# Kernel tuning notes

Measured on AMD Instinct MI355X. Metric: run time of the kernel, lower is better.

Reference implementation:

```python
import jax, jax.numpy as jnp
import numpy as np

EXPERT_CAPACITY = 1024  # per-batch per-expert capacity (token_priority <= capacity)


def setup_inputs() -> dict:
    key = jax.random.key(0)
    ks = jax.random.split(key, 5)
    B, S, D, FF, E = 2, 4096, 1024, 4096, 8
    return {
        "hidden_states": jax.random.normal(ks[0], (B, S, D), dtype=jnp.float32),
        "gate_w": jax.random.normal(ks[1], (D, E), dtype=jnp.float32) * (1.0 / np.sqrt(D)),
        "w1": jax.random.normal(ks[2], (E, D, FF), dtype=jnp.float32) * (1.0 / np.sqrt(D)),
        "w2": jax.random.normal(ks[3], (E, FF, D), dtype=jnp.float32) * (1.0 / np.sqrt(FF)),
        "w3": jax.random.normal(ks[4], (E, D, FF), dtype=jnp.float32) * (1.0 / np.sqrt(D)),
    }


def reference(hidden_states, gate_w, w1, w2, w3):
    B, S, D = hidden_states.shape
    E = gate_w.shape[1]
    C = EXPERT_CAPACITY

    # ---- route (jitter_noise = 0) ----
    router_logits = jnp.einsum("bsd,de->bse", hidden_states, gate_w)  # [B,S,E]
    router_probs = jax.nn.softmax(router_logits, axis=-1)
    sel = jnp.argmax(router_probs, axis=-1)  # [B,S] top-1 expert
    onehot = jax.nn.one_hot(sel, E, dtype=jnp.int32)  # [B,S,E]
    priority = jnp.cumsum(onehot, axis=1)  # cumsum over sequence (dim=-2)
    # position of token in its chosen expert's buffer (0-based)
    pos = jnp.take_along_axis(priority, sel[..., None], axis=-1)[..., 0] - 1  # [B,S]
    keep = pos < C  # token_priority <= expert_capacity
    max_prob = jnp.max(router_probs, axis=-1, keepdims=True)  # [B,S,1]

    # ---- dispatch: scatter kept tokens into [B,E,C,D]; dropped tokens have pos>=C -> mode='drop'
    b_idx = jnp.broadcast_to(jnp.arange(B)[:, None], (B, S))
    buf = jnp.zeros((B, E, C, D), dtype=hidden_states.dtype)
    buf = buf.at[b_idx, sel, pos].set(hidden_states, mode="drop")

    # ---- per-expert gated MLP (grouped GEMM): act(x@w1) * (x@w3) @ w2 ----
    g = jax.nn.silu(jnp.einsum("becd,edf->becf", buf, w1))
    u = jnp.einsum("becd,edf->becf", buf, w3)
    expert_out = jnp.einsum("becf,efd->becd", g * u, w2)  # [B,E,C,D]

    # ---- combine: kept tokens get expert output, dropped tokens keep hidden_states ----
    pos_g = jnp.minimum(pos, C - 1)  # safe gather index for dropped tokens
    gathered = expert_out[b_idx, sel, pos_g]  # [B,S,D]
    next_states = jnp.where(keep[..., None], gathered, hidden_states)
    out = max_prob * next_states  # dropout is identity (p=0)
    return out, router_logits
```

## Files before the change

### kernel.cpp

```cpp
#include <hip/hip_runtime.h>
#include <hip/hip_bf16.h>
#include <stdint.h>

#define B_  2
#define S_  4096
#define D_  1024
#define FF_ 4096
#define E_  8
#define C_  1024

typedef unsigned short u16;
typedef unsigned int   u32;
typedef float f32x4  __attribute__((ext_vector_type(4)));
typedef short bf16x8 __attribute__((ext_vector_type(8)));
typedef u16   u16x8  __attribute__((ext_vector_type(8)));

static __device__ __forceinline__ u16 f2bf(float f) {
    union { float f; u32 u; } v; v.f = f;
    u32 u = v.u;
    u32 r = (u + 0x7FFFu + ((u >> 16) & 1u)) >> 16;
    return (u16)r;
}

static __device__ __forceinline__ void gload_lds16(const u16* g, u16* l) {
    __builtin_amdgcn_global_load_lds(
        (const __attribute__((address_space(1))) u32*)g,
        (__attribute__((address_space(3))) u32*)l, 16, 0, 0);
}

#define BAR()    asm volatile("s_barrier" ::: "memory")
#define WAITV(n) asm volatile("s_waitcnt vmcnt(" #n ")" ::: "memory")
#define WAITL0() do { asm volatile("s_waitcnt lgkmcnt(0)" ::: "memory"); \
                      __builtin_amdgcn_sched_barrier(0); } while (0)

__global__ __launch_bounds__(256) void transpose_cvt(const float* __restrict__ src,
                                                     u16* __restrict__ dst, int K, int N) {
    __shared__ u16 t[64 * 64];
    size_t mat = (size_t)blockIdx.z * K * N;
    int n0 = blockIdx.x * 64, k0 = blockIdx.y * 64;
    int l = threadIdx.x & 63, w = threadIdx.x >> 6;
#pragma unroll
    for (int p = 0; p < 2; ++p) {
        int k = p * 32 + w * 8 + ((l >> 4) << 1);
        int n = (l & 15) * 4;
        float4 v0 = *(const float4*)&src[mat + (size_t)(k0 + k) * N + n0 + n];
        float4 v1 = *(const float4*)&src[mat + (size_t)(k0 + k + 1) * N + n0 + n];
        float a0[4] = {v0.x, v0.y, v0.z, v0.w};
        float a1[4] = {v1.x, v1.y, v1.z, v1.w};
#pragma unroll
        for (int j = 0; j < 4; ++j) {
            int nn = n + j;
            u32 pk = (u32)f2bf(a0[j]) | ((u32)f2bf(a1[j]) << 16);
            int slot = (k >> 3) ^ ((nn & 7) ^ ((nn >> 3) & 7));
            *(u32*)((char*)t + nn * 128 + slot * 16 + (k & 7) * 2) = pk;
        }
    }
    __syncthreads();
#pragma unroll
    for (int p = 0; p < 2; ++p) {
        int n = p * 32 + (threadIdx.x >> 3);
        int k8 = threadIdx.x & 7;
        int slot = k8 ^ ((n & 7) ^ ((n >> 3) & 7));
        u16x8 v = *(u16x8*)((char*)t + n * 128 + slot * 16);
        *(u16x8*)&dst[mat + (size_t)(n0 + n) * K + k0 + k8 * 8] = v;
    }
}

__global__ __launch_bounds__(256) void router_kernel(const float* __restrict__ hidden,
                                                     const float* __restrict__ gate_w,
                                                     float* __restrict__ logits_out,
                                                     int* __restrict__ sel,
                                                     float* __restrict__ maxp) {
    __shared__ float gw[D_ * E_];
    for (int i = threadIdx.x; i < D_ * E_ / 4; i += 256)
        ((float4*)gw)[i] = ((const float4*)gate_w)[i];
    __syncthreads();

    int wave = threadIdx.x >> 6, lane = threadIdx.x & 63;
    int tok = blockIdx.x * 4 + wave;
    const float* hrow = hidden + (size_t)tok * D_;

    double acc[8] = {0, 0, 0, 0, 0, 0, 0, 0};
#pragma unroll 4
    for (int i = 0; i < D_ / 64; i++) {
        int d = i * 64 + lane;
        float h = hrow[d];
        const float4* g4 = (const float4*)(gw + d * 8);
        float4 g0 = g4[0], g1 = g4[1];
        acc[0] += (double)h * g0.x; acc[1] += (double)h * g0.y;
        acc[2] += (double)h * g0.z; acc[3] += (double)h * g0.w;
        acc[4] += (double)h * g1.x; acc[5] += (double)h * g1.y;
        acc[6] += (double)h * g1.z; acc[7] += (double)h * g1.w;
    }
#pragma unroll
    for (int off = 32; off > 0; off >>= 1)
#pragma unroll
        for (int e = 0; e < 8; e++)
            acc[e] += __shfl_xor(acc[e], off);

    float l[8];
#pragma unroll
    for (int e = 0; e < 8; e++) l[e] = (float)acc[e];
    if (lane < 8) logits_out[(size_t)tok * 8 + lane] = l[lane];

    int am = 0; float mx = l[0];
#pragma unroll
    for (int e = 1; e < 8; e++) if (l[e] > mx) { mx = l[e]; am = e; }
    float sum = 0.f;
#pragma unroll
    for (int e = 0; e < 8; e++) sum += expf(l[e] - mx);
    if (lane == 0) { sel[tok] = am; maxp[tok] = 1.0f / sum; }
}

__global__ __launch_bounds__(1024) void scan_kernel(const int* __restrict__ sel,
                                                    int* __restrict__ pos,
                                                    int* __restrict__ slot_token,
                                                    int* __restrict__ counts) {
    __shared__ int hist[16][8];
    __shared__ int base[16][8];
    int b = blockIdx.x;
    int tid = threadIdx.x, wv = tid >> 6, l = tid & 63;
    unsigned long long below = (l == 0) ? 0ull : ((~0ull) >> (64 - l));
    const int* sb = sel + b * S_;

    int eloc[4];
    int cnt[8] = {0, 0, 0, 0, 0, 0, 0, 0};
#pragma unroll
    for (int c = 0; c < 4; c++) {
        int s = wv * 256 + c * 64 + l;
        int e = sb[s];
        eloc[c] = e;
#pragma unroll
        for (int ex = 0; ex < 8; ex++)
            cnt[ex] += (int)__popcll(__ballot(e == ex));
    }
    if (l == 0)
#pragma unroll
        for (int ex = 0; ex < 8; ex++) hist[wv][ex] = cnt[ex];
    __syncthreads();
    if (tid < 128) {
        int ex = tid & 7, v = tid >> 3;
        int s = 0;
        for (int w2 = 0; w2 < v; w2++) s += hist[w2][ex];
        base[v][ex] = s;
        if (v == 15) {
            int tot = s + hist[15][ex];
            counts[b * 8 + ex] = tot < C_ ? tot : C_;
        }
    }
    __syncthreads();
    int carry[8];
#pragma unroll
    for (int ex = 0; ex < 8; ex++) carry[ex] = base[wv][ex];
#pragma unroll
    for (int c = 0; c < 4; c++) {
        int s = wv * 256 + c * 64 + l;
        int e = eloc[c];
        int p = 0;
#pragma unroll
        for (int ex = 0; ex < 8; ex++) {
            unsigned long long m = __ballot(e == ex);
            if (e == ex) p = carry[ex] + (int)__popcll(m & below);
            carry[ex] += (int)__popcll(m);
        }
        pos[b * S_ + s] = p;
        if (p < C_) slot_token[(b * E_ + e) * C_ + p] = s;
    }
}

__global__ __launch_bounds__(256) void gather_kernel(const float* __restrict__ hidden,
                                                     const int* __restrict__ slot_token,
                                                     const int* __restrict__ counts,
                                                     u16* __restrict__ xg) {
    int z = blockIdx.x >> 8;
    int r0 = (blockIdx.x & 255) * 4;
    int cnt = counts[z];
    int slot = r0 + (threadIdx.x >> 6);
    if (slot >= cnt) return;
    int l = threadIdx.x & 63;
    int b = z >> 3;
    int tok = slot_token[z * C_ + slot];
    const float4* src = (const float4*)(hidden + (size_t)(b * S_ + tok) * D_) + l * 4;
    u16x8* dst = (u16x8*)(xg + ((size_t)z * C_ + slot) * D_) + l * 2;
#pragma unroll
    for (int h = 0; h < 2; h++) {
        float4 a = src[h * 2], c = src[h * 2 + 1];
        u16x8 o;
        o[0] = f2bf(a.x); o[1] = f2bf(a.y); o[2] = f2bf(a.z); o[3] = f2bf(a.w);
        o[4] = f2bf(c.x); o[5] = f2bf(c.y); o[6] = f2bf(c.z); o[7] = f2bf(c.w);
        dst[h] = o;
    }
}

__global__ __launch_bounds__(256, 2) void gemm1_kernel(const u16* __restrict__ xg,
                                                       const u16* __restrict__ w1t,
                                                       const u16* __restrict__ w3t,
                                                       const int* __restrict__ counts,
                                                       u16* __restrict__ hbuf) {
    extern __shared__ u16 lds[];
    int phys = blockIdx.x;
    int virt = (phys & 7) * 512 + (phys >> 3);
    int by = virt & 7, bx = (virt >> 3) & 31, bz = virt >> 8;

    int z = bz;
    int cnt = counts[z];
    int c0 = by * 128;
    if (c0 >= cnt) return;
    int n0 = bx * 128;
    int e = z & 7;

    int tid = threadIdx.x, wn = tid >> 6, l = tid & 63;

    const u16* pA[2];
#pragma unroll
    for (int i = 0; i < 2; i++) {
        int q = i * 256 + tid;
        int r = q >> 2, pc = q & 3;
        pA[i] = xg + ((size_t)z * C_ + c0 + r) * D_ + (pc ^ ((r >> 1) & 3)) * 8;
    }
    const u16* pB[4];
#pragma unroll
    for (int i = 0; i < 4; i++) {
        int q = i * 256 + tid;
        int R = q >> 2, pc = q & 3;
        int panel = (R >> 5) & 1;
        int ffl = ((R >> 6) << 5) + (R & 31);
        const u16* wmat = panel ? w3t : w1t;
        pB[i] = wmat + ((size_t)e * FF_ + n0 + ffl) * D_ + (pc ^ ((R >> 1) & 3)) * 8;
    }
    u32 dA = (u32)tid * 8;
    u32 dB = 4096 + (u32)tid * 8;

    u32 ck = (u32)(((l >> 4) ^ ((l >> 1) & 3)) * 8);

    f32x4 acc[8][4] = {};

    auto STAGE = [&](int t) {
        u16* Ls = lds + (t % 3) * 12288;
        int ko = t << 5;
#pragma unroll
        for (int i = 0; i < 2; i++) gload_lds16(pA[i] + ko, Ls + dA + i * 2048);
#pragma unroll
        for (int i = 0; i < 4; i++) gload_lds16(pB[i] + ko, Ls + dB + i * 2048);
    };

    constexpr int NK = D_ / 32;
    STAGE(0); STAGE(1);
    for (int t = 0; t < NK; ++t) {
        if (t + 1 < NK) { WAITV(6); } else { WAITV(0); }
        BAR();
        const u16* Ls = lds + (t % 3) * 12288;
        bf16x8 af[8], bf[4];
#pragma unroll
        for (int f = 0; f < 8; f++)
            af[f] = *(const bf16x8*)(Ls + (u32)(f * 16 + (l & 15)) * 32 + ck);
#pragma unroll
        for (int j = 0; j < 4; j++)
            bf[j] = *(const bf16x8*)(Ls + 4096 + (u32)(wn * 64 + j * 16 + (l & 15)) * 32 + ck);
        if (t + 2 < NK) STAGE(t + 2);
        WAITL0();
        __builtin_amdgcn_s_setprio(1);
#pragma unroll
        for (int f = 0; f < 8; f++)
#pragma unroll
            for (int j = 0; j < 4; j++)
                acc[f][j] = __builtin_amdgcn_mfma_f32_16x16x32_bf16(af[f], bf[j], acc[f][j], 0, 0, 0);
        __builtin_amdgcn_s_setprio(0);
    }

#pragma unroll
    for (int f = 0; f < 8; f++) {
        int rb = c0 + f * 16 + ((l >> 4) << 2);
#pragma unroll
        for (int j = 0; j < 2; j++) {
            int ff = n0 + wn * 32 + j * 16 + (l & 15);
#pragma unroll
            for (int r = 0; r < 4; r++) {
                int slot = rb + r;
                if (slot < cnt) {
                    float g = acc[f][j][r], uu = acc[f][j + 2][r];
                    float h = (g / (1.f + __expf(-g))) * uu;
                    hbuf[((size_t)z * C_ + slot) * FF_ + ff] = f2bf(h);
                }
            }
        }
    }
}

__global__ __launch_bounds__(512, 2) void gemm2_kernel(const u16* __restrict__ hbuf,
                                                       const u16* __restrict__ w2t,
                                                       const int* __restrict__ slot_token,
                                                       const int* __restrict__ counts,
                                                       const float* __restrict__ maxp,
                                                       float* __restrict__ out) {
    extern __shared__ u16 lds[];
    int phys = blockIdx.x + 4 * (blockIdx.y + 4 * blockIdx.z);
    int virt = (phys & 7) * 32 + (phys >> 3);
    int bx = virt & 3, by = (virt >> 2) & 3, bz = virt >> 4;

    int z = bz;
    int cnt = counts[z];
    int c0 = by * 256;
    if (c0 >= cnt) return;
    int n0 = bx * 256;
    int b = z >> 3, e = z & 7;

    int tid = threadIdx.x, w = tid >> 6, l = tid & 63;
    int wm = w >> 2, wn = w & 3;

    int arow0 = tid >> 2;
    int lk = ((tid & 3) ^ ((tid >> 3) & 3)) * 8;
    const u16* pA0 = hbuf + ((size_t)z * C_ + c0 + arow0) * FF_ + lk;
    const u16* pA1 = pA0 + (size_t)128 * FF_;
    const u16* pB0 = w2t + ((size_t)e * D_ + n0 + arow0) * FF_ + lk;
    const u16* pB1 = pB0 + (size_t)128 * FF_;
    u32 wsl = (u32)tid * 8;

    u32 ck  = (u32)(((l >> 4) ^ ((l >> 1) & 3)) * 8);
    u32 aoff = (u32)(wm * 128 + (l & 15)) * 32 + ck;
    u32 boff = 8192 + (u32)(wn * 64 + (l & 15)) * 32 + ck;

    auto STAGE_A = [&](int t) {
        u16* Ls = lds + ((t & 3) << 14);
        int ko = t << 5;
        gload_lds16(pA0 + ko, Ls + wsl);
        gload_lds16(pA1 + ko, Ls + 4096 + wsl);
    };
    auto STAGE_B = [&](int t) {
        u16* Ls = lds + ((t & 3) << 14);
        int ko = t << 5;
        gload_lds16(pB0 + ko, Ls + 8192 + wsl);
        gload_lds16(pB1 + ko, Ls + 12288 + wsl);
    };

    f32x4 acc[8][4] = {};

    constexpr int NK = FF_ / 32;
    STAGE_A(0); STAGE_B(0); STAGE_A(1); STAGE_B(1); STAGE_A(2); STAGE_B(2);
    for (int t = 0; t < NK; ++t) {
        if (t + 2 < NK)      { WAITV(8); }
        else if (t + 1 < NK) { WAITV(4); }
        else                 { WAITV(0); }
        BAR();
        const u16* Ls = lds + ((t & 3) << 14);
        bf16x8 af[8], bfv[4];
#pragma unroll
        for (int f = 0; f < 4; f++) af[f] = *(const bf16x8*)(Ls + aoff + f * 512);
#pragma unroll
        for (int n = 0; n < 4; n++) bfv[n] = *(const bf16x8*)(Ls + boff + n * 512);
        if (t + 3 < NK) STAGE_A(t + 3);
        WAITL0();
        __builtin_amdgcn_s_setprio(1);
#pragma unroll
        for (int f = 0; f < 4; f++)
#pragma unroll
            for (int n = 0; n < 4; n++)
                acc[f][n] = __builtin_amdgcn_mfma_f32_16x16x32_bf16(af[f], bfv[n], acc[f][n], 0, 0, 0);
        __builtin_amdgcn_s_setprio(0);
        BAR();
#pragma unroll
        for (int f = 4; f < 8; f++) af[f] = *(const bf16x8*)(Ls + aoff + f * 512);
        if (t + 3 < NK) STAGE_B(t + 3);
        WAITL0();
        __builtin_amdgcn_s_setprio(1);
#pragma unroll
        for (int f = 4; f < 8; f++)
#pragma unroll
            for (int n = 0; n < 4; n++)
                acc[f][n] = __builtin_amdgcn_mfma_f32_16x16x32_bf16(af[f], bfv[n], acc[f][n], 0, 0, 0);
        __builtin_amdgcn_s_setprio(0);
    }

#pragma unroll
    for (int f = 0; f < 8; f++) {
        int row = wm * 128 + f * 16 + ((l >> 4) << 2);
#pragma unroll
        for (int rr = 0; rr < 4; rr++) {
            int slot = c0 + row + rr;
            if (slot < cnt) {
                int s = slot_token[z * C_ + slot];
                float sc = maxp[b * S_ + s];
                float* orow = out + ((size_t)b * S_ + s) * D_ + n0 + wn * 64 + (l & 15);
#pragma unroll
                for (int n = 0; n < 4; n++)
                    orow[n * 16] = sc * acc[f][n][rr];
            }
        }
    }
}

__global__ __launch_bounds__(256) void combine_dropped(const float* __restrict__ hidden,
                                                       const int* __restrict__ pos,
                                                       const float* __restrict__ maxp,
                                                       float* __restrict__ out) {
    int t = blockIdx.x;
    if (pos[t] < C_) return;
    float sc = maxp[t];
    const float* src = hidden + (size_t)t * D_;
    float* dst = out + (size_t)t * D_;
    for (int d = threadIdx.x; d < D_; d += 256) dst[d] = sc * src[d];
}

extern "C" void kernel_launch(void* const* d_in, const int* in_sizes, int n_in,
                              void* d_out, int out_size, void* d_ws, size_t ws_size,
                              hipStream_t stream) {
    const float* hidden = (const float*)d_in[0];
    const float* gate_w = (const float*)d_in[1];
    const float* w1     = (const float*)d_in[2];
    const float* w2     = (const float*)d_in[3];
    const float* w3     = (const float*)d_in[4];

    float* out        = (float*)d_out;
    float* logits_out = out + (size_t)B_ * S_ * D_;

    char* ws = (char*)d_ws;
    u16* xg        = (u16*)ws;            ws += (size_t)B_ * E_ * C_ * D_ * 2;
    u16* w1t       = (u16*)ws;            ws += (size_t)E_ * D_ * FF_ * 2;
    u16* w3t       = (u16*)ws;            ws += (size_t)E_ * D_ * FF_ * 2;
    u16* w2t       = (u16*)ws;            ws += (size_t)E_ * D_ * FF_ * 2;
    u16* hbuf      = (u16*)ws;            ws += (size_t)B_ * E_ * C_ * FF_ * 2;
    int*   sel        = (int*)ws;         ws += (size_t)B_ * S_ * 4;
    int*   pos        = (int*)ws;         ws += (size_t)B_ * S_ * 4;
    float* maxp       = (float*)ws;       ws += (size_t)B_ * S_ * 4;
    int*   slot_token = (int*)ws;         ws += (size_t)B_ * E_ * C_ * 4;
    int*   counts     = (int*)ws;         ws += (size_t)B_ * E_ * 4;

    (void)hipFuncSetAttribute((const void*)gemm1_kernel,
                              hipFuncAttributeMaxDynamicSharedMemorySize, 73728);
    (void)hipFuncSetAttribute((const void*)gemm2_kernel,
                              hipFuncAttributeMaxDynamicSharedMemorySize, 131072);

    router_kernel<<<B_ * S_ / 4, 256, 0, stream>>>(hidden, gate_w, logits_out, sel, maxp);
    scan_kernel<<<B_, 1024, 0, stream>>>(sel, pos, slot_token, counts);
    gather_kernel<<<B_ * E_ * 256, 256, 0, stream>>>(hidden, slot_token, counts, xg);

    transpose_cvt<<<dim3(FF_ / 64, D_ / 64, E_), 256, 0, stream>>>(w1, w1t, D_, FF_);
    transpose_cvt<<<dim3(FF_ / 64, D_ / 64, E_), 256, 0, stream>>>(w3, w3t, D_, FF_);
    transpose_cvt<<<dim3(D_ / 64, FF_ / 64, E_), 256, 0, stream>>>(w2, w2t, FF_, D_);

    gemm1_kernel<<<4096, 256, 73728, stream>>>(xg, w1t, w3t, counts, hbuf);
    gemm2_kernel<<<dim3(4, 4, 16), 512, 131072, stream>>>(hbuf, w2t, slot_token, counts, maxp, out);
    combine_dropped<<<B_ * S_, 256, 0, stream>>>(hidden, pos, maxp, out);
}
```

Baseline: 474.5 us.

## Make gemm1 a persistent kernel pulling tiles from an atomic work queue

Replaces the fixed 4096-block gemm1 grid with 512 persistent blocks that fetch tile indices from a global atomic counter. The scan kernel resets the counter. Tiles past an expert's token count are skipped cheaply inside the loop instead of costing a block launch. This is meant to improve load balance across CUs and cut launch and tail overhead, but it drops the previous XCD-aware block swizzle, adds atomic contention, and leaves a possible race on the shared item index when a block skips an empty tile.

New measurement: 682.6 us. 43.9% more time.

```diff
diff --git a/kernel.cpp b/kernel.cpp
--- a/kernel.cpp
+++ b/kernel.cpp
@@ -115,11 +115,13 @@
 __global__ __launch_bounds__(1024) void scan_kernel(const int* __restrict__ sel,
                                                     int* __restrict__ pos,
                                                     int* __restrict__ slot_token,
-                                                    int* __restrict__ counts) {
+                                                    int* __restrict__ counts,
+                                                    int* __restrict__ ctr) {
     __shared__ int hist[16][8];
     __shared__ int base[16][8];
     int b = blockIdx.x;
     int tid = threadIdx.x, wv = tid >> 6, l = tid & 63;
+    if (b == 0 && tid == 0) ctr[0] = 0;
     unsigned long long below = (l == 0) ? 0ull : ((~0ull) >> (64 - l));
     const int* sb = sel + b * S_;
 
@@ -192,95 +194,101 @@
     }
 }
 
+#define G1_NITEMS (16 * 32 * 8)
 __global__ __launch_bounds__(256, 2) void gemm1_kernel(const u16* __restrict__ xg,
                                                        const u16* __restrict__ w1t,
                                                        const u16* __restrict__ w3t,
                                                        const int* __restrict__ counts,
-                                                       u16* __restrict__ hbuf) {
+                                                       u16* __restrict__ hbuf,
+                                                       int* __restrict__ ctr) {
     extern __shared__ u16 lds[];
-    int phys = blockIdx.x;
-    int virt = (phys & 7) * 512 + (phys >> 3);
-    int by = virt & 7, bx = (virt >> 3) & 31, bz = virt >> 8;
-
-    int z = bz;
-    int cnt = counts[z];
-    int c0 = by * 128;
-    if (c0 >= cnt) return;
-    int n0 = bx * 128;
-    int e = z & 7;
+    __shared__ int s_item;
 
     int tid = threadIdx.x, wn = tid >> 6, l = tid & 63;
-
-    const u16* pA[2];
-#pragma unroll
-    for (int i = 0; i < 2; i++) {
-        int q = i * 256 + tid;
-        int r = q >> 2, pc = q & 3;
-        pA[i] = xg + ((size_t)z * C_ + c0 + r) * D_ + (pc ^ ((r >> 1) & 3)) * 8;
-    }
-    const u16* pB[4];
-#pragma unroll
-    for (int i = 0; i < 4; i++) {
-        int q = i * 256 + tid;
-        int R = q >> 2, pc = q & 3;
-        int panel = (R >> 5) & 1;
-        int ffl = ((R >> 6) << 5) + (R & 31);
-        const u16* wmat = panel ? w3t : w1t;
-        pB[i] = wmat + ((size_t)e * FF_ + n0 + ffl) * D_ + (pc ^ ((R >> 1) & 3)) * 8;
-    }
+    u32 ck = (u32)(((l >> 4) ^ ((l >> 1) & 3)) * 8);
     u32 dA = (u32)tid * 8;
     u32 dB = 4096 + (u32)tid * 8;
-
-    u32 ck = (u32)(((l >> 4) ^ ((l >> 1) & 3)) * 8);
-
-    f32x4 acc[8][4] = {};
-
-    auto STAGE = [&](int t) {
-        u16* Ls = lds + (t % 3) * 12288;
-        int ko = t << 5;
-#pragma unroll
-        for (int i = 0; i < 2; i++) gload_lds16(pA[i] + ko, Ls + dA + i * 2048);
-#pragma unroll
-        for (int i = 0; i < 4; i++) gload_lds16(pB[i] + ko, Ls + dB + i * 2048);
-    };
-
-    constexpr int NK = D_ / 32;
-    STAGE(0); STAGE(1);
-    for (int t = 0; t < NK; ++t) {
-        if (t + 1 < NK) { WAITV(6); } else { WAITV(0); }
-        BAR();
-        const u16* Ls = lds + (t % 3) * 12288;
-        bf16x8 af[8], bf[4];
-#pragma unroll
-        for (int f = 0; f < 8; f++)
-            af[f] = *(const bf16x8*)(Ls + (u32)(f * 16 + (l & 15)) * 32 + ck);
-#pragma unroll
-        for (int j = 0; j < 4; j++)
-            bf[j] = *(const bf16x8*)(Ls + 4096 + (u32)(wn * 64 + j * 16 + (l & 15)) * 32 + ck);
-        if (t + 2 < NK) STAGE(t + 2);
-        WAITL0();
-        __builtin_amdgcn_s_setprio(1);
-#pragma unroll
-        for (int f = 0; f < 8; f++)
+    int srcxor = ((tid & 3) ^ ((tid >> 3) & 3)) * 8;
+
+    for (;;) {
+        if (tid == 0) s_item = atomicAdd(ctr, 1);
+        __syncthreads();
+        int item = s_item;
+        if (item >= G1_NITEMS) break;
+        int cy = item & 7, ffx = (item >> 3) & 31, z = item >> 8;
+        int cnt = counts[z];
+        int c0 = cy * 128;
+        if (c0 >= cnt) continue;
+        int n0 = ffx * 128;
+        int e = z & 7;
+
+        const u16* pA[2];
+#pragma unroll
+        for (int i = 0; i < 2; i++) {
+            int q = i * 256 + tid;
+            int r = q >> 2;
+            pA[i] = xg + ((size_t)z * C_ + c0 + r) * D_ + srcxor;
+        }
+        const u16* pB[4];
+#pragma unroll
+        for (int i = 0; i < 4; i++) {
+            int q = i * 256 + tid;
+            int R = q >> 2;
+            int panel = (R >> 5) & 1;
+            int ffl = ((R >> 6) << 5) + (R & 31);
+            const u16* wmat = panel ? w3t : w1t;
+            pB[i] = wmat + ((size_t)e * FF_ + n0 + ffl) * D_ + srcxor;
+        }
+
+        f32x4 acc[8][4] = {};
+
+        auto STAGE = [&](int t) {
+            u16* Ls = lds + (t % 3) * 12288;
+            int ko = t << 5;
+#pragma unroll
+            for (int i = 0; i < 2; i++) gload_lds16(pA[i] + ko, Ls + dA + i * 2048);
+#pragma unroll
+            for (int i = 0; i < 4; i++) gload_lds16(pB[i] + ko, Ls + dB + i * 2048);
+        };
+
+        constexpr int NK = D_ / 32;
+        STAGE(0); STAGE(1);
+        for (int t = 0; t < NK; ++t) {
+            if (t + 1 < NK) { WAITV(6); } else { WAITV(0); }
+            BAR();
+            const u16* Ls = lds + (t % 3) * 12288;
+            bf16x8 af[8], bf[4];
+#pragma unroll
+            for (int f = 0; f < 8; f++)
+                af[f] = *(const bf16x8*)(Ls + (u32)(f * 16 + (l & 15)) * 32 + ck);
 #pragma unroll
             for (int j = 0; j < 4; j++)
-                acc[f][j] = __builtin_amdgcn_mfma_f32_16x16x32_bf16(af[f], bf[j], acc[f][j], 0, 0, 0);
-        __builtin_amdgcn_s_setprio(0);
-    }
-
-#pragma unroll
-    for (int f = 0; f < 8; f++) {
-        int rb = c0 + f * 16 + ((l >> 4) << 2);
-#pragma unroll
-        for (int j = 0; j < 2; j++) {
-            int ff = n0 + wn * 32 + j * 16 + (l & 15);
-#pragma unroll
-            for (int r = 0; r < 4; r++) {
-                int slot = rb + r;
-                if (slot < cnt) {
-                    float g = acc[f][j][r], uu = acc[f][j + 2][r];
-                    float h = (g / (1.f + __expf(-g))) * uu;
-                    hbuf[((size_t)z * C_ + slot) * FF_ + ff] = f2bf(h);
+                bf[j] = *(const bf16x8*)(Ls + 4096 + (u32)(wn * 64 + j * 16 + (l & 15)) * 32 + ck);
+            if (t + 2 < NK) STAGE(t + 2);
+            WAITL0();
+            __builtin_amdgcn_s_setprio(1);
+#pragma unroll
+            for (int f = 0; f < 8; f++)
+#pragma unroll
+                for (int j = 0; j < 4; j++)
+                    acc[f][j] = __builtin_amdgcn_mfma_f32_16x16x32_bf16(af[f], bf[j], acc[f][j], 0, 0, 0);
+            __builtin_amdgcn_s_setprio(0);
+        }
+
+#pragma unroll
+        for (int f = 0; f < 8; f++) {
+            int rb = c0 + f * 16 + ((l >> 4) << 2);
+#pragma unroll
+            for (int j = 0; j < 2; j++) {
+                int ff = n0 + wn * 32 + j * 16 + (l & 15);
+#pragma unroll
+                for (int r = 0; r < 4; r++) {
+                    int slot = rb + r;
+                    if (slot < cnt) {
+                        float g = acc[f][j][r], uu = acc[f][j + 2][r];
+                        float h = (g / (1.f + __expf(-g))) * uu;
+                        hbuf[((size_t)z * C_ + slot) * FF_ + ff] = f2bf(h);
+                    }
                 }
             }
         }
@@ -424,6 +432,7 @@
     float* maxp       = (float*)ws;       ws += (size_t)B_ * S_ * 4;
     int*   slot_token = (int*)ws;         ws += (size_t)B_ * E_ * C_ * 4;
     int*   counts     = (int*)ws;         ws += (size_t)B_ * E_ * 4;
+    int*   ctr        = (int*)ws;         ws += 256;
 
     (void)hipFuncSetAttribute((const void*)gemm1_kernel,
                               hipFuncAttributeMaxDynamicSharedMemorySize, 73728);
@@ -431,14 +440,14 @@
                               hipFuncAttributeMaxDynamicSharedMemorySize, 131072);
 
     router_kernel<<<B_ * S_ / 4, 256, 0, stream>>>(hidden, gate_w, logits_out, sel, maxp);
-    scan_kernel<<<B_, 1024, 0, stream>>>(sel, pos, slot_token, counts);
+    scan_kernel<<<B_, 1024, 0, stream>>>(sel, pos, slot_token, counts, ctr);
     gather_kernel<<<B_ * E_ * 256, 256, 0, stream>>>(hidden, slot_token, counts, xg);
 
     transpose_cvt<<<dim3(FF_ / 64, D_ / 64, E_), 256, 0, stream>>>(w1, w1t, D_, FF_);
     transpose_cvt<<<dim3(FF_ / 64, D_ / 64, E_), 256, 0, stream>>>(w3, w3t, D_, FF_);
     transpose_cvt<<<dim3(D_ / 64, FF_ / 64, E_), 256, 0, stream>>>(w2, w2t, FF_, D_);
 
-    gemm1_kernel<<<4096, 256, 73728, stream>>>(xg, w1t, w3t, counts, hbuf);
+    gemm1_kernel<<<512, 256, 73728, stream>>>(xg, w1t, w3t, counts, hbuf, ctr);
     gemm2_kernel<<<dim3(4, 4, 16), 512, 131072, stream>>>(hbuf, w2t, slot_token, counts, maxp, out);
     combine_dropped<<<B_ * S_, 256, 0, stream>>>(hidden, pos, maxp, out);
 }
```

## Enlarge gemm1 tile to 256x128 with 8 waves and k-64 double-buffered phases

Applied to the files above, without the earlier changes.

Rewrites the fused w1/w3 GEMM so each block of 512 threads computes a 256-token by 128-FF tile, with two M-waves sharing the B panel, instead of 128x128 with 4 waves. The K loop now steps by 64 in double-buffered LDS stages split into four phases. Each phase issues loads for the next stage while MFMAs run, and B fragments are reused across two phases. The aim is more reuse of weight loads and less global traffic per FLOP. In exchange it uses more LDS (128KB), allows one block per CU, adds extra barriers per phase, and wastes more work on partially filled capacity tiles.

Result: slower. 515.2 us (+8.6%).

```diff
diff --git a/kernel.cpp b/kernel.cpp
--- a/kernel.cpp
+++ b/kernel.cpp
@@ -192,93 +192,112 @@
     }
 }
 
-__global__ __launch_bounds__(256, 2) void gemm1_kernel(const u16* __restrict__ xg,
+__global__ __launch_bounds__(512, 1) void gemm1_kernel(const u16* __restrict__ xg,
                                                        const u16* __restrict__ w1t,
                                                        const u16* __restrict__ w3t,
                                                        const int* __restrict__ counts,
                                                        u16* __restrict__ hbuf) {
     extern __shared__ u16 lds[];
     int phys = blockIdx.x;
-    int virt = (phys & 7) * 512 + (phys >> 3);
-    int by = virt & 7, bx = (virt >> 3) & 31, bz = virt >> 8;
-
-    int z = bz;
+    int virt = (phys & 7) * 256 + (phys >> 3);
+    int cy = virt & 3, ffx = (virt >> 2) & 31, z = virt >> 7;
+
     int cnt = counts[z];
-    int c0 = by * 128;
+    int c0 = cy * 256;
     if (c0 >= cnt) return;
-    int n0 = bx * 128;
+    int n0 = ffx * 128;
     int e = z & 7;
 
-    int tid = threadIdx.x, wn = tid >> 6, l = tid & 63;
-
+    int tid = threadIdx.x, w = tid >> 6, l = tid & 63;
+    int wm = w >> 2, wn = w & 3;
+
+    int r = tid >> 2;
+    int lc = ((tid & 3) ^ ((tid >> 3) & 3)) * 8;
     const u16* pA[2];
 #pragma unroll
-    for (int i = 0; i < 2; i++) {
-        int q = i * 256 + tid;
-        int r = q >> 2, pc = q & 3;
-        pA[i] = xg + ((size_t)z * C_ + c0 + r) * D_ + (pc ^ ((r >> 1) & 3)) * 8;
-    }
-    const u16* pB[4];
-#pragma unroll
-    for (int i = 0; i < 4; i++) {
-        int q = i * 256 + tid;
-        int R = q >> 2, pc = q & 3;
+    for (int h = 0; h < 2; h++)
+        pA[h] = xg + ((size_t)z * C_ + c0 + h * 128 + r) * D_ + lc;
+    const u16* pB[2];
+#pragma unroll
+    for (int h = 0; h < 2; h++) {
+        int R = h * 128 + r;
         int panel = (R >> 5) & 1;
         int ffl = ((R >> 6) << 5) + (R & 31);
         const u16* wmat = panel ? w3t : w1t;
-        pB[i] = wmat + ((size_t)e * FF_ + n0 + ffl) * D_ + (pc ^ ((R >> 1) & 3)) * 8;
-    }
-    u32 dA = (u32)tid * 8;
-    u32 dB = 4096 + (u32)tid * 8;
+        pB[h] = wmat + ((size_t)e * FF_ + n0 + ffl) * D_ + lc;
+    }
+    u32 dstA = (u32)tid * 8;
+    u32 dstB = 16384 + (u32)tid * 8;
 
     u32 ck = (u32)(((l >> 4) ^ ((l >> 1) & 3)) * 8);
+    u32 aBase = (u32)wm * 8192 + (u32)(l & 15) * 32 + ck;
+    u32 bBase = 16384 + (u32)(wn >> 1) * 8192 + (u32)((wn & 1) * 64 + (l & 15)) * 32 + ck;
 
     f32x4 acc[8][4] = {};
-
-    auto STAGE = [&](int t) {
-        u16* Ls = lds + (t % 3) * 12288;
-        int ko = t << 5;
-#pragma unroll
-        for (int i = 0; i < 2; i++) gload_lds16(pA[i] + ko, Ls + dA + i * 2048);
-#pragma unroll
-        for (int i = 0; i < 4; i++) gload_lds16(pB[i] + ko, Ls + dB + i * 2048);
+    bf16x8 bfr[4];
+
+    auto STAGE = [&](int T, int grp) {
+        u32 buf = ((u32)T & 1) * 32768;
+        int kk = grp >> 1;
+        int ko = (T << 6) + (kk << 5);
+        if ((grp & 1) == 0) {
+#pragma unroll
+            for (int h = 0; h < 2; h++)
+                gload_lds16(pA[h] + ko, lds + buf + (u32)h * 8192 + (u32)kk * 4096 + dstA);
+        } else {
+#pragma unroll
+            for (int h = 0; h < 2; h++)
+                gload_lds16(pB[h] + ko, lds + buf + (u32)h * 8192 + (u32)kk * 4096 + dstB);
+        }
     };
 
-    constexpr int NK = D_ / 32;
-    STAGE(0); STAGE(1);
-    for (int t = 0; t < NK; ++t) {
-        if (t + 1 < NK) { WAITV(6); } else { WAITV(0); }
-        BAR();
-        const u16* Ls = lds + (t % 3) * 12288;
-        bf16x8 af[8], bf[4];
-#pragma unroll
-        for (int f = 0; f < 8; f++)
-            af[f] = *(const bf16x8*)(Ls + (u32)(f * 16 + (l & 15)) * 32 + ck);
-#pragma unroll
-        for (int j = 0; j < 4; j++)
-            bf[j] = *(const bf16x8*)(Ls + 4096 + (u32)(wn * 64 + j * 16 + (l & 15)) * 32 + ck);
-        if (t + 2 < NK) STAGE(t + 2);
-        WAITL0();
-        __builtin_amdgcn_s_setprio(1);
-#pragma unroll
-        for (int f = 0; f < 8; f++)
-#pragma unroll
-            for (int j = 0; j < 4; j++)
-                acc[f][j] = __builtin_amdgcn_mfma_f32_16x16x32_bf16(af[f], bf[j], acc[f][j], 0, 0, 0);
-        __builtin_amdgcn_s_setprio(0);
+    constexpr int NT = D_ / 64;
+    STAGE(0, 0); STAGE(0, 1); STAGE(0, 2); STAGE(0, 3);
+
+    for (int T = 0; T < NT; ++T) {
+        u32 buf = ((u32)T & 1) * 32768;
+        bool st = (T + 1 < NT);
+#pragma unroll
+        for (int ph = 0; ph < 4; ph++) {
+            int kk = ph >> 1, fh = ph & 1;
+            if (ph == 0) { WAITV(4); }
+            else if (ph == 2) { if (st) { WAITV(4); } else { WAITV(0); } }
+            BAR();
+            const u16* Lk = lds + buf + (u32)kk * 4096;
+            bf16x8 af[4];
+#pragma unroll
+            for (int f = 0; f < 4; f++)
+                af[f] = *(const bf16x8*)(Lk + aBase + (u32)(fh * 4 + f) * 512);
+            if (fh == 0) {
+#pragma unroll
+                for (int j = 0; j < 4; j++)
+                    bfr[j] = *(const bf16x8*)(Lk + bBase + (u32)j * 512);
+            }
+            if (st) STAGE(T + 1, ph);
+            WAITL0();
+            __builtin_amdgcn_s_setprio(1);
+#pragma unroll
+            for (int f = 0; f < 4; f++)
+#pragma unroll
+                for (int j = 0; j < 4; j++)
+                    acc[fh * 4 + f][j] = __builtin_amdgcn_mfma_f32_16x16x32_bf16(
+                        af[f], bfr[j], acc[fh * 4 + f][j], 0, 0, 0);
+            __builtin_amdgcn_s_setprio(0);
+            BAR();
+        }
     }
 
 #pragma unroll
     for (int f = 0; f < 8; f++) {
-        int rb = c0 + f * 16 + ((l >> 4) << 2);
+        int rb = c0 + wm * 128 + f * 16 + ((l >> 4) << 2);
 #pragma unroll
         for (int j = 0; j < 2; j++) {
             int ff = n0 + wn * 32 + j * 16 + (l & 15);
 #pragma unroll
-            for (int r = 0; r < 4; r++) {
-                int slot = rb + r;
+            for (int rr = 0; rr < 4; rr++) {
+                int slot = rb + rr;
                 if (slot < cnt) {
-                    float g = acc[f][j][r], uu = acc[f][j + 2][r];
+                    float g = acc[f][j][rr], uu = acc[f][j + 2][rr];
                     float h = (g / (1.f + __expf(-g))) * uu;
                     hbuf[((size_t)z * C_ + slot) * FF_ + ff] = f2bf(h);
                 }
@@ -426,7 +445,7 @@
     int*   counts     = (int*)ws;         ws += (size_t)B_ * E_ * 4;
 
     (void)hipFuncSetAttribute((const void*)gemm1_kernel,
-                              hipFuncAttributeMaxDynamicSharedMemorySize, 73728);
+                              hipFuncAttributeMaxDynamicSharedMemorySize, 131072);
     (void)hipFuncSetAttribute((const void*)gemm2_kernel,
                               hipFuncAttributeMaxDynamicSharedMemorySize, 131072);
 
@@ -438,7 +457,7 @@
     transpose_cvt<<<dim3(FF_ / 64, D_ / 64, E_), 256, 0, stream>>>(w3, w3t, D_, FF_);
     transpose_cvt<<<dim3(D_ / 64, FF_ / 64, E_), 256, 0, stream>>>(w2, w2t, FF_, D_);
 
-    gemm1_kernel<<<4096, 256, 73728, stream>>>(xg, w1t, w3t, counts, hbuf);
+    gemm1_kernel<<<2048, 512, 131072, stream>>>(xg, w1t, w3t, counts, hbuf);
     gemm2_kernel<<<dim3(4, 4, 16), 512, 131072, stream>>>(hbuf, w2t, slot_token, counts, maxp, out);
     combine_dropped<<<B_ * S_, 256, 0, stream>>>(hidden, pos, maxp, out);
 }
```
